# Kernel optimization log

Hardware: AMD Instinct MI355X
Metric: run time of the kernel (lower is better)

The kernel has to match this reference:

```python
import jax, jax.numpy as jnp
import numpy as np

N_EMBD = 1024
N_HEAD = 16

def setup_inputs() -> dict:
    key = jax.random.key(0)
    ks = jax.random.split(key, 5)
    s = 0.02
    return {
        "x": jax.random.normal(ks[0], (4, 2048, N_EMBD), dtype=jnp.float32),
        "w_attn": jax.random.normal(ks[1], (N_EMBD, 3 * N_EMBD), dtype=jnp.float32) * s,
        "b_attn": jnp.zeros((3 * N_EMBD,), dtype=jnp.float32),
        "w_proj": jax.random.normal(ks[2], (N_EMBD, N_EMBD), dtype=jnp.float32) * s,
        "b_proj": jnp.zeros((N_EMBD,), dtype=jnp.float32),
    }

def reference(x, w_attn, b_attn, w_proj, b_proj):
    B, T, C = x.shape
    H = N_HEAD
    D = C // H
    qkv = x @ w_attn + b_attn                       # [B,T,3C]
    q, k, v = jnp.split(qkv, 3, axis=-1)
    # [B,H,T,D]
    q = q.reshape(B, T, H, D).transpose(0, 2, 1, 3)
    k = k.reshape(B, T, H, D).transpose(0, 2, 1, 3)
    v = v.reshape(B, T, H, D).transpose(0, 2, 1, 3)
    scale = 1.0 / jnp.sqrt(jnp.asarray(D, dtype=x.dtype))
    attn = jnp.einsum("bhqd,bhkd->bhqk", q, k) * scale
    mask = jnp.tril(jnp.ones((T, T), dtype=bool))
    attn = jnp.where(mask, attn, jnp.asarray(-jnp.inf, dtype=attn.dtype))
    attn = jax.nn.softmax(attn, axis=-1)
    out = jnp.einsum("bhqk,bhkd->bhqd", attn, v)    # [B,H,T,D]
    out = out.transpose(0, 2, 1, 3).reshape(B, T, C)
    return out @ w_proj + b_proj
```

## Files before the change

kernel.cpp:

```cpp
#include <hip/hip_runtime.h>


typedef unsigned short u16b;
typedef __bf16 bf16x8 __attribute__((ext_vector_type(8)));
typedef float f32x4 __attribute__((ext_vector_type(4)));
typedef float f32x16 __attribute__((ext_vector_type(16)));
typedef unsigned short u16x4 __attribute__((ext_vector_type(4)));

#define AS1(p) ((const __attribute__((address_space(1))) void*)(p))
#define AS3(p) ((__attribute__((address_space(3))) void*)(p))
#define GLDS(g, l) __builtin_amdgcn_global_load_lds(AS1(g), AS3(l), 16, 0, 0)

__device__ __forceinline__ u16b bfr(float v) {
  union { float f; unsigned u; } x; x.f = v;
  unsigned r = x.u + 0x7fffu + ((x.u >> 16) & 1u);
  return (u16b)(r >> 16);
}

__device__ __forceinline__ unsigned pk2(float lo, float hi) {
  union { __bf16 h[2]; unsigned u; } t;
  t.h[0] = (__bf16)lo; t.h[1] = (__bf16)hi;
  return t.u;
}

__device__ __forceinline__ float max16(const f32x16& v) {
  float a0 = fmaxf(v[0], v[1]), a1 = fmaxf(v[2], v[3]);
  float a2 = fmaxf(v[4], v[5]), a3 = fmaxf(v[6], v[7]);
  float b0 = fmaxf(v[8], v[9]), b1 = fmaxf(v[10], v[11]);
  float b2 = fmaxf(v[12], v[13]), b3 = fmaxf(v[14], v[15]);
  float c0 = fmaxf(a0, a1), c1 = fmaxf(a2, a3);
  float c2 = fmaxf(b0, b1), c3 = fmaxf(b2, b3);
  return fmaxf(fmaxf(c0, c1), fmaxf(c2, c3));
}

__device__ __forceinline__ float sum16(const f32x16& v) {
  float a0 = v[0] + v[1], a1 = v[2] + v[3], a2 = v[4] + v[5], a3 = v[6] + v[7];
  float b0 = v[8] + v[9], b1 = v[10] + v[11], b2 = v[12] + v[13], b3 = v[14] + v[15];
  float c0 = a0 + a1, c1 = a2 + a3, c2 = b0 + b1, c3 = b2 + b3;
  return (c0 + c1) + (c2 + c3);
}

__global__ __launch_bounds__(256) void cvt_bf16_kernel(
    const float* __restrict__ src, u16b* __restrict__ dst, int n4) {
  int i = blockIdx.x * 256 + threadIdx.x;
  const int stride = gridDim.x * 256;
  for (; i < n4; i += stride) {
    const float4 v = reinterpret_cast<const float4*>(src)[i];
    u16x4 o;
    o[0] = bfr(v.x); o[1] = bfr(v.y); o[2] = bfr(v.z); o[3] = bfr(v.w);
    reinterpret_cast<u16x4*>(dst)[i] = o;
  }
}

__global__ __launch_bounds__(256) void transpose_cvt_kernel(
    const float* __restrict__ src, u16b* __restrict__ dst, int R, int C) {
  __shared__ u16b tile[64][72];
  const int nc = C >> 6;
  const int br = blockIdx.x / nc, bc = blockIdx.x % nc;
  const int r0 = br << 6, c0 = bc << 6;
  const int c = threadIdx.x & 63, r4 = threadIdx.x >> 6;
  #pragma unroll
  for (int i = 0; i < 16; ++i) {
    const int r = r4 + 4 * i;
    tile[r][c] = bfr(src[(size_t)(r0 + r) * C + c0 + c]);
  }
  __syncthreads();
  #pragma unroll
  for (int i = 0; i < 16; ++i) {
    const int rr = r4 + 4 * i;
    dst[(size_t)(c0 + rr) * R + r0 + c] = tile[c][rr];
  }
}

template <int EPI>
__global__ __launch_bounds__(256, 2) void gemm128_kernel(
    const u16b* __restrict__ A, const u16b* __restrict__ Bt,
    const float* __restrict__ bias,
    u16b* __restrict__ oQ, u16b* __restrict__ oK, u16b* __restrict__ oVt,
    float* __restrict__ oF, int M, int N, int K) {
  __shared__ u16b smem[16384];
  const int tid = threadIdx.x;
  const int wid = tid >> 6, lane = tid & 63;
  const int nb = N >> 7;
  const int lin = (blockIdx.x & 7) * ((int)gridDim.x >> 3) + (blockIdx.x >> 3);
  const int brow = lin / nb, bcol = lin % nb;
  const int wr = (wid >> 1) << 6, wc = (wid & 1) << 6;

  f32x4 acc[4][4] = {};

  const int ar = (wid << 4) + (lane >> 2);
  const int acs = (((lane & 3) ^ ((lane >> 3) & 3))) << 3;
  const u16b* Ab = A + (size_t)((brow << 7) + ar) * K + acs;
  const u16b* Bb = Bt + (size_t)((bcol << 7) + ar) * K + acs;
  const int fr = lane & 15;
  const int pcs = (((lane >> 4) ^ ((fr >> 1) & 3))) << 4;
  const int nk = K >> 5;

#define STAGE(bufi, kk)                                                        \
  {                                                                            \
    char* sb = (char*)smem + (bufi) * 16384;                                   \
    GLDS(Ab + (kk),                  sb + wid * 1024);                         \
    GLDS(Ab + (size_t)64 * K + (kk), sb + 4096 + wid * 1024);                  \
    GLDS(Bb + (kk),                  sb + 8192 + wid * 1024);                  \
    GLDS(Bb + (size_t)64 * K + (kk), sb + 12288 + wid * 1024);                 \
  }

  STAGE(0, 0);
  STAGE(1, 32);

  #pragma unroll 1
  for (int kt = 0; kt < nk; ++kt) {
    if (kt + 1 < nk) asm volatile("s_waitcnt vmcnt(4)" ::: "memory");
    else             asm volatile("s_waitcnt vmcnt(0)" ::: "memory");
    __builtin_amdgcn_s_barrier();

    const char* As = (const char*)smem + (kt & 1) * 16384;
    const char* Bs = As + 8192;
    bf16x8 af[4], bfv[4];
    #pragma unroll
    for (int i = 0; i < 4; ++i)
      af[i] = *(const bf16x8*)(As + (wr + i * 16 + fr) * 64 + pcs);
    #pragma unroll
    for (int j = 0; j < 4; ++j)
      bfv[j] = *(const bf16x8*)(Bs + (wc + j * 16 + fr) * 64 + pcs);
    __builtin_amdgcn_s_setprio(1);
    #pragma unroll
    for (int i = 0; i < 4; ++i)
      #pragma unroll
      for (int j = 0; j < 4; ++j)
        acc[i][j] = __builtin_amdgcn_mfma_f32_16x16x32_bf16(af[i], bfv[j], acc[i][j], 0, 0, 0);
    __builtin_amdgcn_s_setprio(0);

    __builtin_amdgcn_s_barrier();
    if (kt + 2 < nk) STAGE(kt & 1, (kt + 2) << 5);
  }
#undef STAGE

  const int fq = lane >> 4;
  if (EPI == 1) {
    #pragma unroll
    for (int j = 0; j < 4; ++j) {
      const int n0 = (bcol << 7) + wc + j * 16 + fr;
      const float bv = bias[n0];
      #pragma unroll
      for (int i = 0; i < 4; ++i) {
        #pragma unroll
        for (int r = 0; r < 4; ++r) {
          const int m0 = (brow << 7) + wr + i * 16 + fq * 4 + r;
          oF[(size_t)m0 * N + n0] = acc[i][j][r] + bv;
        }
      }
    }
  } else {
    const int sect = bcol >> 3;
    if (sect < 2) {
      const float qs = (sect == 0) ? 0.1803368801f : 1.0f;
      u16b* oPtr = (sect == 0) ? oQ : oK;
      u16b* tile = (u16b*)smem;
      #pragma unroll
      for (int j = 0; j < 4; ++j) {
        const int n = wc + j * 16 + fr;
        const float bv = bias[(bcol << 7) + n];
        #pragma unroll
        for (int i = 0; i < 4; ++i) {
          #pragma unroll
          for (int r = 0; r < 4; ++r) {
            const int m = wr + i * 16 + fq * 4 + r;
            const int byteoff = m * 256 + (((n >> 3) ^ (m & 7)) << 4) + ((n & 7) << 1);
            *(u16b*)((char*)tile + byteoff) = bfr((acc[i][j][r] + bv) * qs);
          }
        }
      }
      __syncthreads();
      const int nh = wid >> 1;
      const int c = lane & 7;
      #pragma unroll
      for (int it = 0; it < 8; ++it) {
        const int m = ((wid & 1) << 6) + (it << 3) + (lane >> 3);
        const int chunk = (nh << 3) + (c ^ (m & 7));
        const bf16x8 val = *(const bf16x8*)((const char*)tile + m * 256 + chunk * 16);
        const int m0 = (brow << 7) + m;
        const int n0 = (bcol << 7) + (nh << 6) + (c << 3);
        const int bb = m0 >> 11, tt = m0 & 2047;
        const int h = (n0 >> 6) & 15, d = n0 & 63;
        *(bf16x8*)(oPtr + (((size_t)(bb * 16 + h) * 2048 + tt) * 64 + d)) = val;
      }
    } else {
      u16b* tile = (u16b*)smem;
      #pragma unroll
      for (int j = 0; j < 4; ++j) {
        const int nl = wc + j * 16 + fr;
        const float bv = bias[(bcol << 7) + nl];
        #pragma unroll
        for (int i = 0; i < 4; ++i) {
          #pragma unroll
          for (int r = 0; r < 4; ++r) {
            const int m = wr + i * 16 + fq * 4 + r;
            const int byteoff = nl * 256 + (((m >> 3) ^ (nl & 7)) << 4) + ((m & 7) << 1);
            *(u16b*)((char*)tile + byteoff) = bfr(acc[i][j][r] + bv);
          }
        }
      }
      __syncthreads();
      const int row0 = wid << 5;
      const int c16 = lane & 15;
      const int rr = lane >> 4;
      const int t0 = (brow << 7) & 2047;
      const int bb = brow >> 4;
      #pragma unroll
      for (int it = 0; it < 8; ++it) {
        const int nl = row0 + (it << 2) + rr;
        const int pch = c16 ^ (nl & 7);
        const bf16x8 val = *(const bf16x8*)((const char*)tile + nl * 256 + pch * 16);
        const int h = ((bcol & 7) << 1) + (nl >> 6);
        const int d = nl & 63;
        *(bf16x8*)(oVt + ((size_t)((bb << 4) + h) * 64 + d) * 2048 + t0 + (c16 << 3)) = val;
      }
    }
  }
}

__global__ __launch_bounds__(256, 4) void flash_kernel(
    const u16b* __restrict__ Q, const u16b* __restrict__ K,
    const u16b* __restrict__ Vt, u16b* __restrict__ O) {
  __shared__ u16b smem[16384];
  const int bid = blockIdx.x;
  const int bh = bid & 63;
  const int qt = 15 - (bid >> 6);
  const int tid = threadIdx.x, wid = tid >> 6, lane = tid & 63;
  const int ln31 = lane & 31, hi = lane >> 5;
  const int l7 = ln31 & 7;
  const size_t baseQK = (size_t)bh * 2048 * 64;
  const size_t baseV = (size_t)bh * 64 * 2048;
  const int b = bh >> 4, h = bh & 15;
  const int srow = wid * 8 + (lane >> 3);
  const int sc = ((lane & 7) ^ (srow & 7)) << 3;

  const int q0w = (qt << 7) + wid * 32;
  const int NT = 2 * qt + 2;
  const int LT = q0w >> 6;

#define FSTAGE(kt, bi)                                                         \
  {                                                                            \
    char* kb_ = (char*)smem + (bi) * 16384;                                    \
    const int k0_ = (kt) << 6;                                                 \
    GLDS(K + baseQK + (size_t)(k0_ + srow) * 64 + sc,        kb_ + wid * 1024);\
    GLDS(K + baseQK + (size_t)(k0_ + 32 + srow) * 64 + sc,   kb_ + 4096 + wid * 1024);\
    GLDS(Vt + baseV + (size_t)srow * 2048 + k0_ + sc,        kb_ + 8192 + wid * 1024);\
    GLDS(Vt + baseV + (size_t)(32 + srow) * 2048 + k0_ + sc, kb_ + 12288 + wid * 1024);\
  }

  bf16x8 qf[4];
  {
    const u16b* qp = Q + baseQK + (size_t)(q0w + ln31) * 64 + hi * 8;
    #pragma unroll
    for (int kk = 0; kk < 4; ++kk) qf[kk] = *(const bf16x8*)(qp + kk * 16);
  }

  float m_run = -3e38f, l_run = 0.f;
  f32x16 oa0 = {}, oa1 = {};

  FSTAGE(0, 0);
  FSTAGE(1, 1);

  #pragma unroll 1
  for (int kt = 0; kt < NT; ++kt) {
    if (kt + 1 < NT) asm volatile("s_waitcnt vmcnt(4)" ::: "memory");
    else             asm volatile("s_waitcnt vmcnt(0)" ::: "memory");
    __builtin_amdgcn_s_barrier();

    if (kt <= LT) {
      const char* kb = (const char*)smem + (kt & 1) * 16384;
      const char* vb = kb + 8192;
      const bool diag = (kt == LT);
      const int maxsub = diag ? (wid & 1) : 1;

      f32x16 s[2] = {};
      __builtin_amdgcn_s_setprio(1);
      #pragma unroll
      for (int ss = 0; ss < 2; ++ss) {
        if (ss <= maxsub) {
          const int row = 32 * ss + ln31;
          #pragma unroll
          for (int kk = 0; kk < 4; ++kk) {
            const int ch = (2 * kk + hi) ^ (row & 7);
            const bf16x8 kf = *(const bf16x8*)(kb + row * 128 + ch * 16);
            s[ss] = __builtin_amdgcn_mfma_f32_32x32x16_bf16(kf, qf[kk], s[ss], 0, 0, 0);
          }
        }
      }
      __builtin_amdgcn_s_setprio(0);

      if (diag) {
        #pragma unroll
        for (int ss = 0; ss < 2; ++ss) {
          if (ss == (wid & 1)) {
            #pragma unroll
            for (int r = 0; r < 16; ++r) {
              const int kvr = (r & 3) + 8 * (r >> 2) + 4 * hi;
              if (kvr > ln31) s[ss][r] = -3e38f;
            }
          }
        }
      }

      float tm = -3e38f;
      #pragma unroll
      for (int ss = 0; ss < 2; ++ss)
        if (ss <= maxsub) tm = fmaxf(tm, max16(s[ss]));
      tm = fmaxf(tm, __shfl_xor(tm, 32));

      if (!__all(tm <= m_run + 8.f)) {
        const float mnew = fmaxf(m_run, tm);
        const float scale = __builtin_amdgcn_exp2f(m_run - mnew);
        m_run = mnew;
        l_run *= scale;
        #pragma unroll
        for (int r = 0; r < 16; ++r) { oa0[r] *= scale; oa1[r] *= scale; }
      }

      float rs = 0.f;
      #pragma unroll
      for (int ss = 0; ss < 2; ++ss) {
        if (ss <= maxsub) {
          #pragma unroll
          for (int r = 0; r < 16; ++r)
            s[ss][r] = __builtin_amdgcn_exp2f(s[ss][r] - m_run);
          rs += sum16(s[ss]);
        }
      }
      rs += __shfl_xor(rs, 32);
      l_run += rs;

      union WB { unsigned u[4]; bf16x8 v; };
      __builtin_amdgcn_s_setprio(1);
      #pragma unroll
      for (int ss = 0; ss < 2; ++ss) {
        if (ss <= maxsub) {
          WB pA, pB;
#define MKPA(W0, W1, W2, W3, P0, P1, P2, P3, P4, P5, P6, P7)                 \
          {                                                                   \
            unsigned a0 = pk2(P0, P1), a1 = pk2(P2, P3);                      \
            unsigned b0 = pk2(P4, P5), b1 = pk2(P6, P7);                      \
            auto r0 = __builtin_amdgcn_permlane32_swap(a0, b0, false, false); \
            auto r1 = __builtin_amdgcn_permlane32_swap(a1, b1, false, false); \
            unsigned o0[2], o1[2];                                            \
            __builtin_memcpy(o0, &r0, 8); __builtin_memcpy(o1, &r1, 8);       \
            W0 = o0[0]; W2 = o0[1]; W1 = o1[0]; W3 = o1[1];                   \
          }
          MKPA(pA.u[0], pA.u[1], pA.u[2], pA.u[3],
               s[ss][0], s[ss][1], s[ss][2], s[ss][3],
               s[ss][4], s[ss][5], s[ss][6], s[ss][7]);
          MKPA(pB.u[0], pB.u[1], pB.u[2], pB.u[3],
               s[ss][8], s[ss][9], s[ss][10], s[ss][11],
               s[ss][12], s[ss][13], s[ss][14], s[ss][15]);
#undef MKPA
          const int r0v = ln31, r1v = 32 + ln31;
          const int cxa0 = ((2 * ss + hi) ^ (r0v & 7)) << 4;
          const int cxa1 = ((2 * ss + hi) ^ (r1v & 7)) << 4;
          const int cxb0 = ((2 * ss + 1 - hi + hi * 1 + 0) , 0);
          (void)cxb0;
          const int cb0 = (((2 * (ss) + 0) , 0)); (void)cb0;
          const int sl_b = 2 * ss + 1;
          const int cxB0 = ((2 * sl_b + hi - 2 * ss - hi) , 0); (void)cxB0;
          const int chB0 = ((2 * sl_b + hi) ^ (r0v & 7)) << 4;
          const int chB1 = ((2 * sl_b + hi) ^ (r1v & 7)) << 4;
          const char* v0 = vb + r0v * 128;
          const char* v1 = vb + r1v * 128;
          const int chA0 = ((4 * ss + hi) ^ (r0v & 7)) << 4;
          const int chA1 = ((4 * ss + hi) ^ (r1v & 7)) << 4;
          const int chBB0 = ((4 * ss + 2 + hi) ^ (r0v & 7)) << 4;
          const int chBB1 = ((4 * ss + 2 + hi) ^ (r1v & 7)) << 4;
          (void)cxa0; (void)cxa1; (void)chB0; (void)chB1;
          oa0 = __builtin_amdgcn_mfma_f32_32x32x16_bf16(*(const bf16x8*)(v0 + chA0), pA.v, oa0, 0, 0, 0);
          oa1 = __builtin_amdgcn_mfma_f32_32x32x16_bf16(*(const bf16x8*)(v1 + chA1), pA.v, oa1, 0, 0, 0);
          oa0 = __builtin_amdgcn_mfma_f32_32x32x16_bf16(*(const bf16x8*)(v0 + chBB0), pB.v, oa0, 0, 0, 0);
          oa1 = __builtin_amdgcn_mfma_f32_32x32x16_bf16(*(const bf16x8*)(v1 + chBB1), pB.v, oa1, 0, 0, 0);
        }
      }
      __builtin_amdgcn_s_setprio(0);
    }

    __builtin_amdgcn_s_barrier();
    if (kt + 2 < NT) FSTAGE(kt + 2, kt & 1);
  }

  const float inv = 1.0f / l_run;
  const int q = q0w + ln31;
  u16b* orow = O + (size_t)(b * 2048 + q) * 1024 + h * 64;
  #pragma unroll
  for (int rq = 0; rq < 4; ++rq) {
    u16x4 v0, v1;
    #pragma unroll
    for (int j = 0; j < 4; ++j) {
      v0[j] = bfr(oa0[4 * rq + j] * inv);
      v1[j] = bfr(oa1[4 * rq + j] * inv);
    }
    const int d0 = 8 * rq + 4 * hi;
    *(u16x4*)(orow + d0) = v0;
    *(u16x4*)(orow + 32 + d0) = v1;
  }
#undef FSTAGE
}

extern "C" void kernel_launch(void* const* d_in, const int* in_sizes, int n_in,
                              void* d_out, int out_size, void* d_ws, size_t ws_size,
                              hipStream_t stream) {
  const float* x      = (const float*)d_in[0];
  const float* w_attn = (const float*)d_in[1];
  const float* b_attn = (const float*)d_in[2];
  const float* w_proj = (const float*)d_in[3];
  const float* b_proj = (const float*)d_in[4];
  float* out = (float*)d_out;
  char* ws = (char*)d_ws;

  u16b* xb  = (u16b*)(ws + 0);
  u16b* waT = (u16b*)(ws + 16777216);
  u16b* wpT = (u16b*)(ws + 23068672);
  u16b* Qb  = (u16b*)(ws + 25165824);
  u16b* Kb  = (u16b*)(ws + 41943040);
  u16b* Vtb = (u16b*)(ws + 75497472);
  u16b* attn = xb;

  cvt_bf16_kernel<<<2048, 256, 0, stream>>>(x, xb, (8192 * 1024) / 4);
  transpose_cvt_kernel<<<16 * 48, 256, 0, stream>>>(w_attn, waT, 1024, 3072);
  transpose_cvt_kernel<<<16 * 16, 256, 0, stream>>>(w_proj, wpT, 1024, 1024);
  gemm128_kernel<0><<<64 * 24, 256, 0, stream>>>(xb, waT, b_attn, Qb, Kb, Vtb, nullptr,
                                                 8192, 3072, 1024);
  flash_kernel<<<1024, 256, 0, stream>>>(Qb, Kb, Vtb, attn);
  gemm128_kernel<1><<<64 * 8, 256, 0, stream>>>(attn, wpT, b_proj, nullptr, nullptr, nullptr,
                                                out, 8192, 1024, 1024);
}
```

Measured before the change: 175.5 us.

## Deepen GEMM K-tile to 64 and remap blocks for XCD-local L2 reuse

The GEMM kernel now stages a 64-wide K slice per iteration instead of 32. Shared memory doubles to 64 KB, with 8 async global-to-LDS loads per stage and a new 8-chunk XOR swizzle, which halves the number of barrier and wait rounds. The block-to-tile mapping is also rewritten so each XCD owns a contiguous band of 8 row tiles and walks column tiles in groups of 8, aiming to improve L2 reuse of A and B. The doubled LDS per block may reduce occupancy below the requested 2 blocks per CU, and the new mapping hardcodes the grid shape. The flash kernel only loses dead variables.

```diff
diff --git a/kernel.cpp b/kernel.cpp
--- a/kernel.cpp
+++ b/kernel.cpp
@@ -78,65 +78,81 @@
     const float* __restrict__ bias,
     u16b* __restrict__ oQ, u16b* __restrict__ oK, u16b* __restrict__ oVt,
     float* __restrict__ oF, int M, int N, int K) {
-  __shared__ u16b smem[16384];
+  __shared__ u16b smem[32768];
   const int tid = threadIdx.x;
   const int wid = tid >> 6, lane = tid & 63;
-  const int nb = N >> 7;
-  const int lin = (blockIdx.x & 7) * ((int)gridDim.x >> 3) + (blockIdx.x >> 3);
-  const int brow = lin / nb, bcol = lin % nb;
+  const int xcd = blockIdx.x & 7;
+  const int idx = blockIdx.x >> 3;
+  const int stg = idx >> 6, rr6 = idx & 63;
+  const int brow = (xcd << 3) + (rr6 >> 3);
+  const int bcol = (stg << 3) + (rr6 & 7);
   const int wr = (wid >> 1) << 6, wc = (wid & 1) << 6;
 
   f32x4 acc[4][4] = {};
 
-  const int ar = (wid << 4) + (lane >> 2);
-  const int acs = (((lane & 3) ^ ((lane >> 3) & 3))) << 3;
-  const u16b* Ab = A + (size_t)((brow << 7) + ar) * K + acs;
-  const u16b* Bb = Bt + (size_t)((bcol << 7) + ar) * K + acs;
+  const int srow = (wid << 5) + (lane >> 3);
+  const int sc = ((lane & 7) ^ (lane >> 3)) << 3;
+  const u16b* Ab = A + (size_t)((brow << 7) + srow) * K + sc;
+  const u16b* Bb = Bt + (size_t)((bcol << 7) + srow) * K + sc;
   const int fr = lane & 15;
-  const int pcs = (((lane >> 4) ^ ((fr >> 1) & 3))) << 4;
-  const int nk = K >> 5;
+  const int fq = lane >> 4;
+  const int pcs0 = ((fq) ^ (fr & 7)) << 4;
+  const int pcs1 = ((4 + fq) ^ (fr & 7)) << 4;
+  const int nk = K >> 6;
 
 #define STAGE(bufi, kk)                                                        \
   {                                                                            \
-    char* sb = (char*)smem + (bufi) * 16384;                                   \
-    GLDS(Ab + (kk),                  sb + wid * 1024);                         \
-    GLDS(Ab + (size_t)64 * K + (kk), sb + 4096 + wid * 1024);                  \
-    GLDS(Bb + (kk),                  sb + 8192 + wid * 1024);                  \
-    GLDS(Bb + (size_t)64 * K + (kk), sb + 12288 + wid * 1024);                 \
+    char* sb = (char*)smem + (bufi) * 32768;                                   \
+    _Pragma("unroll")                                                          \
+    for (int j = 0; j < 4; ++j)                                                \
+      GLDS(Ab + (size_t)8 * K * j + (kk), sb + wid * 4096 + j * 1024);         \
+    _Pragma("unroll")                                                          \
+    for (int j = 0; j < 4; ++j)                                                \
+      GLDS(Bb + (size_t)8 * K * j + (kk), sb + 16384 + wid * 4096 + j * 1024); \
   }
 
   STAGE(0, 0);
-  STAGE(1, 32);
+  STAGE(1, 64);
 
   #pragma unroll 1
   for (int kt = 0; kt < nk; ++kt) {
-    if (kt + 1 < nk) asm volatile("s_waitcnt vmcnt(4)" ::: "memory");
+    if (kt + 1 < nk) asm volatile("s_waitcnt vmcnt(8)" ::: "memory");
     else             asm volatile("s_waitcnt vmcnt(0)" ::: "memory");
     __builtin_amdgcn_s_barrier();
 
-    const char* As = (const char*)smem + (kt & 1) * 16384;
-    const char* Bs = As + 8192;
-    bf16x8 af[4], bfv[4];
+    const char* As = (const char*)smem + (kt & 1) * 32768;
+    const char* Bs = As + 16384;
+    bf16x8 af0[4], af1[4], bf0[4], bf1[4];
+    #pragma unroll
+    for (int i = 0; i < 4; ++i) {
+      const int rowb = (wr + i * 16 + fr) * 128;
+      af0[i] = *(const bf16x8*)(As + rowb + pcs0);
+      af1[i] = *(const bf16x8*)(As + rowb + pcs1);
+    }
+    #pragma unroll
+    for (int j = 0; j < 4; ++j) {
+      const int rowb = (wc + j * 16 + fr) * 128;
+      bf0[j] = *(const bf16x8*)(Bs + rowb + pcs0);
+      bf1[j] = *(const bf16x8*)(Bs + rowb + pcs1);
+    }
+    __builtin_amdgcn_s_setprio(1);
     #pragma unroll
     for (int i = 0; i < 4; ++i)
-      af[i] = *(const bf16x8*)(As + (wr + i * 16 + fr) * 64 + pcs);
-    #pragma unroll
-    for (int j = 0; j < 4; ++j)
-      bfv[j] = *(const bf16x8*)(Bs + (wc + j * 16 + fr) * 64 + pcs);
-    __builtin_amdgcn_s_setprio(1);
+      #pragma unroll
+      for (int j = 0; j < 4; ++j)
+        acc[i][j] = __builtin_amdgcn_mfma_f32_16x16x32_bf16(af0[i], bf0[j], acc[i][j], 0, 0, 0);
     #pragma unroll
     for (int i = 0; i < 4; ++i)
       #pragma unroll
       for (int j = 0; j < 4; ++j)
-        acc[i][j] = __builtin_amdgcn_mfma_f32_16x16x32_bf16(af[i], bfv[j], acc[i][j], 0, 0, 0);
+        acc[i][j] = __builtin_amdgcn_mfma_f32_16x16x32_bf16(af1[i], bf1[j], acc[i][j], 0, 0, 0);
     __builtin_amdgcn_s_setprio(0);
 
     __builtin_amdgcn_s_barrier();
-    if (kt + 2 < nk) STAGE(kt & 1, (kt + 2) << 5);
+    if (kt + 2 < nk) STAGE(kt & 1, (kt + 2) << 6);
   }
 #undef STAGE
 
-  const int fq = lane >> 4;
   if (EPI == 1) {
     #pragma unroll
     for (int j = 0; j < 4; ++j) {
@@ -204,12 +220,12 @@
       __syncthreads();
       const int row0 = wid << 5;
       const int c16 = lane & 15;
-      const int rr = lane >> 4;
+      const int rw = lane >> 4;
       const int t0 = (brow << 7) & 2047;
       const int bb = brow >> 4;
       #pragma unroll
       for (int it = 0; it < 8; ++it) {
-        const int nl = row0 + (it << 2) + rr;
+        const int nl = row0 + (it << 2) + rw;
         const int pch = c16 ^ (nl & 7);
         const bf16x8 val = *(const bf16x8*)((const char*)tile + nl * 256 + pch * 16);
         const int h = ((bcol & 7) << 1) + (nl >> 6);
@@ -229,7 +245,6 @@
   const int qt = 15 - (bid >> 6);
   const int tid = threadIdx.x, wid = tid >> 6, lane = tid & 63;
   const int ln31 = lane & 31, hi = lane >> 5;
-  const int l7 = ln31 & 7;
   const size_t baseQK = (size_t)bh * 2048 * 64;
   const size_t baseV = (size_t)bh * 64 * 2048;
   const int b = bh >> 4, h = bh & 15;
@@ -356,26 +371,16 @@
                s[ss][12], s[ss][13], s[ss][14], s[ss][15]);
 #undef MKPA
           const int r0v = ln31, r1v = 32 + ln31;
-          const int cxa0 = ((2 * ss + hi) ^ (r0v & 7)) << 4;
-          const int cxa1 = ((2 * ss + hi) ^ (r1v & 7)) << 4;
-          const int cxb0 = ((2 * ss + 1 - hi + hi * 1 + 0) , 0);
-          (void)cxb0;
-          const int cb0 = (((2 * (ss) + 0) , 0)); (void)cb0;
-          const int sl_b = 2 * ss + 1;
-          const int cxB0 = ((2 * sl_b + hi - 2 * ss - hi) , 0); (void)cxB0;
-          const int chB0 = ((2 * sl_b + hi) ^ (r0v & 7)) << 4;
-          const int chB1 = ((2 * sl_b + hi) ^ (r1v & 7)) << 4;
           const char* v0 = vb + r0v * 128;
           const char* v1 = vb + r1v * 128;
           const int chA0 = ((4 * ss + hi) ^ (r0v & 7)) << 4;
           const int chA1 = ((4 * ss + hi) ^ (r1v & 7)) << 4;
-          const int chBB0 = ((4 * ss + 2 + hi) ^ (r0v & 7)) << 4;
-          const int chBB1 = ((4 * ss + 2 + hi) ^ (r1v & 7)) << 4;
-          (void)cxa0; (void)cxa1; (void)chB0; (void)chB1;
+          const int chB0 = ((4 * ss + 2 + hi) ^ (r0v & 7)) << 4;
+          const int chB1 = ((4 * ss + 2 + hi) ^ (r1v & 7)) << 4;
           oa0 = __builtin_amdgcn_mfma_f32_32x32x16_bf16(*(const bf16x8*)(v0 + chA0), pA.v, oa0, 0, 0, 0);
           oa1 = __builtin_amdgcn_mfma_f32_32x32x16_bf16(*(const bf16x8*)(v1 + chA1), pA.v, oa1, 0, 0, 0);
-          oa0 = __builtin_amdgcn_mfma_f32_32x32x16_bf16(*(const bf16x8*)(v0 + chBB0), pB.v, oa0, 0, 0, 0);
-          oa1 = __builtin_amdgcn_mfma_f32_32x32x16_bf16(*(const bf16x8*)(v1 + chBB1), pB.v, oa1, 0, 0, 0);
+          oa0 = __builtin_amdgcn_mfma_f32_32x32x16_bf16(*(const bf16x8*)(v0 + chB0), pB.v, oa0, 0, 0, 0);
+          oa1 = __builtin_amdgcn_mfma_f32_32x32x16_bf16(*(const bf16x8*)(v1 + chB1), pB.v, oa1, 0, 0, 0);
         }
       }
       __builtin_amdgcn_s_setprio(0);
```

Measured after the change: 166.3 us. -5.3%, faster.
